# Kernel optimization log

Measured on AMD Instinct MI355X. Metric: run time of the kernel, lower is better.

Reference implementation:

```python
import jax, jax.numpy as jnp
import numpy as np

# skimage color deconvolution constants: hed_from_rgb = inv(rgb_from_hed)
_RGB_FROM_HED = np.array([[0.65, 0.70, 0.29],
                          [0.07, 0.99, 0.11],
                          [0.27, 0.57, 0.78]], dtype=np.float64)
_HED_FROM_RGB = np.linalg.inv(_RGB_FROM_HED).astype(np.float32)
_LOG_ADJUST = float(np.log(1e-6))  # skimage separate_stains log base


def setup_inputs() -> dict:
    key = jax.random.key(0)
    k1, = jax.random.split(key, 1)
    x = jax.random.uniform(k1, (64, 3, 512, 512), dtype=jnp.float32)  # RGB patches in [0,1]
    gamma = jnp.ones((1,), dtype=jnp.float32)   # InstanceNorm2d affine weight
    beta = jnp.zeros((1,), dtype=jnp.float32)   # InstanceNorm2d affine bias
    return {"x": x, "gamma": gamma, "beta": beta}


def reference(x, gamma, beta):
    h_weights = jnp.asarray(_HED_FROM_RGB[:, 0])  # only H (hematoxylin) column needed, shape (3,)

    # --- skimage.color.separate_stains, batched (replaces per-sample CPU loop) ---
    rgb = jnp.clip(x, 0.0, 1.0)                  # torch.clamp(t, 0, 1)
    rgb = jnp.maximum(rgb, 1e-6)                 # avoid log(0)
    od = jnp.log(rgb) / _LOG_ADJUST              # optical density, (B,3,H,W)
    h = jnp.einsum('bchw,c->bhw', od, h_weights) # stain matrix multiply, H channel only
    h = jnp.maximum(h, 0.0)[:, None, :, :]       # (B,1,H,W), skimage clips stains at 0

    # --- FFT magnitude spectrum ---
    fft = jnp.fft.fft2(h, norm='forward')        # complex64, scaled by 1/(H*W)
    fft = jnp.fft.fftshift(fft, axes=(-2, -1))
    mag = jnp.abs(fft)

    # --- _normalize_log_fft: log1p then per-image min-max ---
    log_mag = jnp.log1p(mag)
    mn = jnp.min(log_mag, axis=(-2, -1), keepdims=True)
    mx = jnp.max(log_mag, axis=(-2, -1), keepdims=True)
    rng = mx - mn
    safe_rng = jnp.where(rng > 0, rng, 1.0)
    normed = jnp.where(rng > 0, (log_mag - mn) / safe_rng, 0.0)

    # --- nn.InstanceNorm2d(1, affine=True), eps=1e-5 ---
    mu = jnp.mean(normed, axis=(-2, -1), keepdims=True)
    var = jnp.var(normed, axis=(-2, -1), keepdims=True)
    out = (normed - mu) * jax.lax.rsqrt(var + 1e-5)
    return out * gamma[None, :, None, None] + beta[None, :, None, None]
```

## Files before the change

kernel.cpp:

```cpp
#include <hip/hip_runtime.h>
#include <hip/hip_fp16.h>
#include <math.h>


#define PI_F 3.14159265358979323846f
#define FROW 264
#define LMSTR 264
#define LVMAX 1.6f
#define QE (65535.0f / LVMAX)
#define QD (LVMAX / 65535.0f)
#define XSTR 568

__device__ __forceinline__ int MU(int p) {
    return ((p >> 6) * 72) + (p & 56) + ((p & 7) ^ ((p >> 3) & 7));
}
__device__ __forceinline__ int odrev(int k) {
    return ((k & 7) << 6) | (k & 56) | (k >> 6);
}

__device__ __forceinline__ float2 cadd(float2 a, float2 b) { return make_float2(a.x + b.x, a.y + b.y); }
__device__ __forceinline__ float2 csub(float2 a, float2 b) { return make_float2(a.x - b.x, a.y - b.y); }
__device__ __forceinline__ float2 cmul(float2 a, float2 w) {
    return make_float2(a.x * w.x - a.y * w.y, a.x * w.y + a.y * w.x);
}

__device__ __forceinline__ void dft8(float2 v[8]) {
    const float s = 0.70710678118654752f;
    float2 a0 = cadd(v[0], v[4]), b0 = csub(v[0], v[4]);
    float2 a1 = cadd(v[1], v[5]), b1 = csub(v[1], v[5]);
    float2 a2 = cadd(v[2], v[6]), b2 = csub(v[2], v[6]);
    float2 a3 = cadd(v[3], v[7]), b3 = csub(v[3], v[7]);
    b1 = make_float2(s * (b1.x + b1.y), s * (b1.y - b1.x));
    b2 = make_float2(b2.y, -b2.x);
    b3 = make_float2(s * (b3.y - b3.x), -s * (b3.x + b3.y));
    float2 c0 = cadd(a0, a2), c1 = cadd(a1, a3);
    float2 d0 = csub(a0, a2), d1 = csub(a1, a3);
    d1 = make_float2(d1.y, -d1.x);
    v[0] = cadd(c0, c1); v[4] = csub(c0, c1);
    v[2] = cadd(d0, d1); v[6] = csub(d0, d1);
    float2 e0 = cadd(b0, b2), e1 = cadd(b1, b3);
    float2 f0 = csub(b0, b2), f1 = csub(b1, b3);
    f1 = make_float2(f1.y, -f1.x);
    v[1] = cadd(e0, e1); v[5] = csub(e0, e1);
    v[3] = cadd(f0, f1); v[7] = csub(f0, f1);
}

__device__ __forceinline__ void fft512_reg(float2* Xw, const float2* TW, int lane) {
    float2 v[8];
    #pragma unroll
    for (int m = 0; m < 8; ++m) v[m] = Xw[MU(lane + (m << 6))];
    dft8(v);
    #pragma unroll
    for (int m = 1; m < 8; ++m) v[m] = cmul(v[m], TW[(lane * m) & 511]);
    #pragma unroll
    for (int m = 0; m < 8; ++m) Xw[MU((m << 6) + lane)] = v[m];
    __builtin_amdgcn_wave_barrier();
    const int b = lane >> 3, t = lane & 7;
    const int base2 = (b << 6) + t;
    #pragma unroll
    for (int m = 0; m < 8; ++m) v[m] = Xw[MU(base2 + (m << 3))];
    dft8(v);
    #pragma unroll
    for (int m = 1; m < 8; ++m) v[m] = cmul(v[m], TW[(t * m) << 3]);
    #pragma unroll
    for (int m = 0; m < 8; ++m) Xw[MU(base2 + (m << 3))] = v[m];
    __builtin_amdgcn_wave_barrier();
    const int base3 = (b << 6) + (t << 3);
    #pragma unroll
    for (int j = 0; j < 8; ++j) v[j] = Xw[MU(base3 + j)];
    dft8(v);
    #pragma unroll
    for (int sidx = 0; sidx < 8; ++sidx) Xw[MU(base3 + sidx)] = v[sidx];
    __builtin_amdgcn_wave_barrier();
}

__device__ __forceinline__ void hstore(float2* Xw, int c,
                                       float r0v, float g0v, float b0v,
                                       float r1v, float g1v, float b1v,
                                       float w0, float w1, float w2) {
    r0v = fminf(fmaxf(r0v, 1e-6f), 1.0f);
    g0v = fminf(fmaxf(g0v, 1e-6f), 1.0f);
    b0v = fminf(fmaxf(b0v, 1e-6f), 1.0f);
    r1v = fminf(fmaxf(r1v, 1e-6f), 1.0f);
    g1v = fminf(fmaxf(g1v, 1e-6f), 1.0f);
    b1v = fminf(fmaxf(b1v, 1e-6f), 1.0f);
    float h0 = fmaxf(w0 * __log2f(r0v) + w1 * __log2f(g0v) + w2 * __log2f(b0v), 0.0f);
    float h1 = fmaxf(w0 * __log2f(r1v) + w1 * __log2f(g1v) + w2 * __log2f(b1v), 0.0f);
    Xw[MU(c)] = make_float2(h0, h1);
}

__global__ __launch_bounds__(256) void k_rowfft(const float* __restrict__ x,
                                                __half2* __restrict__ Fh,
                                                float w0, float w1, float w2) {
    const int b = blockIdx.x >> 6;
    const int p = blockIdx.x & 63;
    __shared__ float2 X[4 * XSTR];
    __shared__ float2 TW[512];
    const int tid = threadIdx.x;
    const int w = tid >> 6, lane = tid & 63;
    #pragma unroll
    for (int t = 0; t < 8; ++t) {
        int idx = lane + (t << 6);
        float sn, cs;
        __sincosf(-PI_F * (float)idx * (1.0f / 256.0f), &sn, &cs);
        TW[idx] = make_float2(cs, sn);
    }
    float2* Xw = X + w * XSTR;
    const float* xb = x + (size_t)b * 786432;
    const int r0 = (p << 3) + (w << 1);

    #pragma unroll
    for (int q = 0; q < 2; ++q) {
        const int cb = (q << 8) + (lane << 2);
        float4 R0 = *(const float4*)(xb +          (r0 << 9) + cb);
        float4 G0 = *(const float4*)(xb + 262144 + (r0 << 9) + cb);
        float4 B0 = *(const float4*)(xb + 524288 + (r0 << 9) + cb);
        float4 R1 = *(const float4*)(xb +          ((r0 + 1) << 9) + cb);
        float4 G1 = *(const float4*)(xb + 262144 + ((r0 + 1) << 9) + cb);
        float4 B1 = *(const float4*)(xb + 524288 + ((r0 + 1) << 9) + cb);
        hstore(Xw, cb + 0, R0.x, G0.x, B0.x, R1.x, G1.x, B1.x, w0, w1, w2);
        hstore(Xw, cb + 1, R0.y, G0.y, B0.y, R1.y, G1.y, B1.y, w0, w1, w2);
        hstore(Xw, cb + 2, R0.z, G0.z, B0.z, R1.z, G1.z, B1.z, w0, w1, w2);
        hstore(Xw, cb + 3, R0.w, G0.w, B0.w, R1.w, G1.w, B1.w, w0, w1, w2);
    }
    __builtin_amdgcn_wave_barrier();

    fft512_reg(Xw, TW, lane);

    __half2* Fb = Fh + (size_t)b * (512 * FROW);
    #pragma unroll
    for (int t = 0; t < 4; ++t) {
        int k = lane + (t << 6);
        int m = (512 - k) & 511;
        float2 zk = Xw[MU(odrev(k))];
        float2 zm = Xw[MU(odrev(m))];
        Fb[r0 * FROW + k]       = __floats2half2_rn(0.5f * (zk.x + zm.x),  0.5f * (zk.y - zm.y));
        Fb[(r0 + 1) * FROW + k] = __floats2half2_rn(0.5f * (zk.y + zm.y), -0.5f * (zk.x - zm.x));
    }
    if (lane == 0) {
        float2 z = Xw[MU(odrev(256))];
        Fb[r0 * FROW + 256]       = __floats2half2_rn(z.x, 0.0f);
        Fb[(r0 + 1) * FROW + 256] = __floats2half2_rn(z.y, 0.0f);
    }
}

__global__ __launch_bounds__(512) void k_colfft(const __half2* __restrict__ Fh,
                                                unsigned short* __restrict__ lmu,
                                                float4* __restrict__ partials) {
    const int b = blockIdx.x >> 4;
    const int g = blockIdx.x & 15;
    __shared__ float2 X[8 * XSTR];
    __shared__ float2 TW[512];
    __shared__ float4 wred[8];
    const int tid = threadIdx.x;
    const int w = tid >> 6, lane = tid & 63;
    {
        float sn, cs;
        __sincosf(-PI_F * (float)tid * (1.0f / 256.0f), &sn, &cs);
        TW[tid] = make_float2(cs, sn);
    }
    const __half2* Fb = Fh + (size_t)b * (512 * FROW);
    unsigned short* lm_b = lmu + (size_t)b * (512 * LMSTR);
    float mn = 1e30f, mx = -1e30f, s1 = 0.0f, s2 = 0.0f;

    for (int pass = 0; pass < 2; ++pass) {
        const int u0 = (g << 4) + (pass << 3);
        const bool packpass = (g == 0 && pass == 0);
        __syncthreads();
        for (int i = tid; i < 4096; i += 512) {
            int y = i >> 3, c = i & 7;
            float2 v;
            if (packpass && c == 0) {
                float2 f0   = __half22float2(Fb[y * FROW]);
                float2 f256 = __half22float2(Fb[y * FROW + 256]);
                v = make_float2(f0.x, f256.x);
            } else {
                v = __half22float2(Fb[y * FROW + u0 + c]);
            }
            X[c * XSTR + MU(y)] = v;
        }
        __syncthreads();
        fft512_reg(X + w * XSTR, TW, lane);
        __syncthreads();
        for (int i = tid; i < 4096; i += 512) {
            int k = i >> 3, c = i & 7;
            int ro = (k + 256) & 511;
            if (packpass && c == 0) {
                int m = (512 - k) & 511;
                float2 zk = X[MU(odrev(k))];
                float2 zm = X[MU(odrev(m))];
                float2 c0   = make_float2(0.5f * (zk.x + zm.x),  0.5f * (zk.y - zm.y));
                float2 c256 = make_float2(0.5f * (zk.y + zm.y), -0.5f * (zk.x - zm.x));
                float lv0   = __log2f(1.0f + sqrtf(c0.x * c0.x + c0.y * c0.y));
                float lv256 = __log2f(1.0f + sqrtf(c256.x * c256.x + c256.y * c256.y));
                unsigned q0 = (unsigned)__float2uint_rn(fminf(lv0,   LVMAX) * QE);
                unsigned q6 = (unsigned)__float2uint_rn(fminf(lv256, LVMAX) * QE);
                lm_b[ro * LMSTR]       = (unsigned short)q0;
                lm_b[ro * LMSTR + 256] = (unsigned short)q6;
                mn = fminf(mn, fminf(lv0, lv256));
                mx = fmaxf(mx, fmaxf(lv0, lv256));
                s1 += lv0 + lv256;
                s2 += lv0 * lv0 + lv256 * lv256;
            } else {
                int u = u0 + c;
                float2 v = X[c * XSTR + MU(odrev(k))];
                float lv = __log2f(1.0f + sqrtf(v.x * v.x + v.y * v.y));
                unsigned q = (unsigned)__float2uint_rn(fminf(lv, LVMAX) * QE);
                lm_b[ro * LMSTR + u] = (unsigned short)q;
                mn = fminf(mn, lv);
                mx = fmaxf(mx, lv);
                s1 += 2.0f * lv;
                s2 += 2.0f * lv * lv;
            }
        }
    }

    #pragma unroll
    for (int off = 32; off > 0; off >>= 1) {
        mn = fminf(mn, __shfl_down(mn, off, 64));
        mx = fmaxf(mx, __shfl_down(mx, off, 64));
        s1 += __shfl_down(s1, off, 64);
        s2 += __shfl_down(s2, off, 64);
    }
    if (lane == 0) wred[w] = make_float4(mn, mx, s1, s2);
    __syncthreads();
    if (tid == 0) {
        float4 r = wred[0];
        #pragma unroll
        for (int wv = 1; wv < 8; ++wv) {
            float4 q2 = wred[wv];
            r.x = fminf(r.x, q2.x);
            r.y = fmaxf(r.y, q2.y);
            r.z += q2.z;
            r.w += q2.w;
        }
        partials[blockIdx.x] = r;
    }
}

__global__ __launch_bounds__(64) void k_coeff(const float4* __restrict__ partials,
                                              const float* __restrict__ gamma,
                                              const float* __restrict__ beta,
                                              float2* __restrict__ coeff) {
    const int b = blockIdx.x;
    float mn = 1e30f, mx = -1e30f, s1 = 0.0f, s2 = 0.0f;
    if (threadIdx.x < 16) {
        float4 r = partials[(b << 4) + threadIdx.x];
        mn = r.x; mx = r.y; s1 = r.z; s2 = r.w;
    }
    #pragma unroll
    for (int off = 32; off > 0; off >>= 1) {
        mn = fminf(mn, __shfl_down(mn, off, 64));
        mx = fmaxf(mx, __shfl_down(mx, off, 64));
        s1 += __shfl_down(s1, off, 64);
        s2 += __shfl_down(s2, off, 64);
    }
    if (threadIdx.x == 0) {
        const float N = 262144.0f;
        float mean = s1 / N;
        float var = fmaxf(s2 / N - mean * mean, 0.0f);
        float rng = mx - mn;
        float g = gamma[0], bt = beta[0];
        float A, B;
        if (rng > 0.0f) {
            float inv = 1.0f / rng;
            float varn = var * inv * inv;
            float sc = 1.0f / sqrtf(varn + 1e-5f);
            A = g * sc * inv;
            B = bt - mean * A;
        } else {
            A = 0.0f;
            B = bt;
        }
        coeff[b] = make_float2(A, B);
    }
}

__global__ __launch_bounds__(256) void k_norm(const unsigned short* __restrict__ lmu,
                                              float* __restrict__ out,
                                              const float2* __restrict__ coeff) {
    const int p = blockIdx.x & 255;
    const int b = blockIdx.x >> 8;
    const float2 ab = coeff[b];
    const float A = ab.x, B = ab.y;
    const int rA = p;
    const int rB = (p == 0) ? 256 : 512 - p;
    const unsigned short* lb = lmu + (size_t)b * (512 * LMSTR);
    float* ob = out + ((size_t)b << 18);
    const int tid = threadIdx.x;
    #pragma unroll
    for (int hh = 0; hh < 2; ++hh) {
        const int r = hh ? rB : rA;
        const int rm = (512 - r) & 511;
        const unsigned short* Ld = lb + (size_t)r * LMSTR;
        const unsigned short* Lm = lb + (size_t)rm * LMSTR;
        float lvd = (float)Ld[tid] * QD;
        ob[(r << 9) + 256 + tid] = A * lvd + B;
        float lvm = (tid == 0) ? ((float)Ld[256] * QD)
                               : ((float)Lm[256 - tid] * QD);
        ob[(r << 9) + tid] = A * lvm + B;
    }
}

extern "C" void kernel_launch(void* const* d_in, const int* in_sizes, int n_in,
                              void* d_out, int out_size, void* d_ws, size_t ws_size,
                              hipStream_t stream) {
    const float* x     = (const float*)d_in[0];
    const float* gamma = (const float*)d_in[1];
    const float* beta  = (const float*)d_in[2];
    float* out = (float*)d_out;

    __half2* Fh = (__half2*)d_ws;
    unsigned short* lmu = (unsigned short*)((char*)d_ws + ((size_t)40 << 20));
    float4* partials = (float4*)((char*)d_ws + ((size_t)60 << 20));
    float2* coeff    = (float2*)((char*)d_ws + ((size_t)60 << 20) + 1024 * sizeof(float4));

    const double M00=0.65, M01=0.70, M02=0.29;
    const double M10=0.07, M11=0.99, M12=0.11;
    const double M20=0.27, M21=0.57, M22=0.78;
    const double det = M00*(M11*M22 - M12*M21)
                     - M01*(M10*M22 - M12*M20)
                     + M02*(M10*M21 - M11*M20);
    const float hw0 = (float)( (M11*M22 - M12*M21) / det);
    const float hw1 = (float)(-(M10*M22 - M12*M20) / det);
    const float hw2 = (float)( (M10*M21 - M11*M20) / det);
    const float invLA2 = (float)(log(2.0) / log(1e-6));
    const float sN = 1.0f / (512.0f * 512.0f);
    const float w0 = hw0 * invLA2 * sN;
    const float w1 = hw1 * invLA2 * sN;
    const float w2 = hw2 * invLA2 * sN;

    k_rowfft<<<64 * 64, 256, 0, stream>>>(x, Fh, w0, w1, w2);
    k_colfft<<<64 * 16, 512, 0, stream>>>(Fh, lmu, partials);
    k_coeff<<<64, 64, 0, stream>>>(partials, gamma, beta, coeff);
    k_norm<<<64 * 256, 256, 0, stream>>>(lmu, out, coeff);
}
```

Measured before the change: 118.3 us.

## Fuse coefficient reduction into column FFT via last-block ticket; tile normalize kernel

Removes the separate k_coeff launch by having the last k_colfft block to finish, detected with an atomic ticket and threadfence, compute the per-image normalization coefficients. A hipMemsetAsync resets the ticket before each launch. k_norm is restructured so each block stages 8 rows of quantized log-magnitude in shared memory and writes float4-vectorized outputs, cutting the block count from 16384 to 4096. This trades a kernel launch for an atomic and a memset, and the shared-memory staging adds a barrier per block.

```diff
diff --git a/kernel.cpp b/kernel.cpp
--- a/kernel.cpp
+++ b/kernel.cpp
@@ -146,12 +146,17 @@
 
 __global__ __launch_bounds__(512) void k_colfft(const __half2* __restrict__ Fh,
                                                 unsigned short* __restrict__ lmu,
-                                                float4* __restrict__ partials) {
+                                                float4* __restrict__ partials,
+                                                float2* __restrict__ coeff,
+                                                unsigned int* __restrict__ ticket,
+                                                const float* __restrict__ gamma,
+                                                const float* __restrict__ beta) {
     const int b = blockIdx.x >> 4;
     const int g = blockIdx.x & 15;
     __shared__ float2 X[8 * XSTR];
     __shared__ float2 TW[512];
     __shared__ float4 wred[8];
+    __shared__ int isLastS;
     const int tid = threadIdx.x;
     const int w = tid >> 6, lane = tid & 63;
     {
@@ -235,70 +240,95 @@
             r.w += q2.w;
         }
         partials[blockIdx.x] = r;
-    }
-}
-
-__global__ __launch_bounds__(64) void k_coeff(const float4* __restrict__ partials,
-                                              const float* __restrict__ gamma,
-                                              const float* __restrict__ beta,
-                                              float2* __restrict__ coeff) {
-    const int b = blockIdx.x;
-    float mn = 1e30f, mx = -1e30f, s1 = 0.0f, s2 = 0.0f;
-    if (threadIdx.x < 16) {
-        float4 r = partials[(b << 4) + threadIdx.x];
-        mn = r.x; mx = r.y; s1 = r.z; s2 = r.w;
-    }
-    #pragma unroll
-    for (int off = 32; off > 0; off >>= 1) {
-        mn = fminf(mn, __shfl_down(mn, off, 64));
-        mx = fmaxf(mx, __shfl_down(mx, off, 64));
-        s1 += __shfl_down(s1, off, 64);
-        s2 += __shfl_down(s2, off, 64);
-    }
-    if (threadIdx.x == 0) {
-        const float N = 262144.0f;
-        float mean = s1 / N;
-        float var = fmaxf(s2 / N - mean * mean, 0.0f);
-        float rng = mx - mn;
-        float g = gamma[0], bt = beta[0];
-        float A, B;
-        if (rng > 0.0f) {
-            float inv = 1.0f / rng;
-            float varn = var * inv * inv;
-            float sc = 1.0f / sqrtf(varn + 1e-5f);
-            A = g * sc * inv;
-            B = bt - mean * A;
-        } else {
-            A = 0.0f;
-            B = bt;
-        }
-        coeff[b] = make_float2(A, B);
+        __threadfence();
+        unsigned old = atomicAdd(ticket, 1u);
+        isLastS = (old == 1023u);
+    }
+    __syncthreads();
+    if (isLastS) {
+        __threadfence();
+        if (tid < 64) {
+            float fmn = 1e30f, fmx = -1e30f, fs1 = 0.0f, fs2 = 0.0f;
+            #pragma unroll
+            for (int k = 0; k < 16; ++k) {
+                float4 r = partials[(tid << 4) + k];
+                fmn = fminf(fmn, r.x);
+                fmx = fmaxf(fmx, r.y);
+                fs1 += r.z;
+                fs2 += r.w;
+            }
+            const float N = 262144.0f;
+            float mean = fs1 / N;
+            float var = fmaxf(fs2 / N - mean * mean, 0.0f);
+            float rng = fmx - fmn;
+            float gm = gamma[0], bt = beta[0];
+            float A, B;
+            if (rng > 0.0f) {
+                float inv = 1.0f / rng;
+                float varn = var * inv * inv;
+                float sc = 1.0f / sqrtf(varn + 1e-5f);
+                A = gm * sc * inv;
+                B = bt - mean * A;
+            } else {
+                A = 0.0f;
+                B = bt;
+            }
+            coeff[tid] = make_float2(A, B);
+        }
     }
 }
 
 __global__ __launch_bounds__(256) void k_norm(const unsigned short* __restrict__ lmu,
                                               float* __restrict__ out,
                                               const float2* __restrict__ coeff) {
-    const int p = blockIdx.x & 255;
-    const int b = blockIdx.x >> 8;
+    const int j = blockIdx.x & 63;
+    const int b = blockIdx.x >> 6;
+    __shared__ unsigned short L[8][260];
     const float2 ab = coeff[b];
     const float A = ab.x, B = ab.y;
-    const int rA = p;
-    const int rB = (p == 0) ? 256 : 512 - p;
     const unsigned short* lb = lmu + (size_t)b * (512 * LMSTR);
     float* ob = out + ((size_t)b << 18);
     const int tid = threadIdx.x;
-    #pragma unroll
-    for (int hh = 0; hh < 2; ++hh) {
-        const int r = hh ? rB : rA;
-        const int rm = (512 - r) & 511;
+
+    auto rowOf = [&](int row8) -> int {
+        int q = row8 >> 1, h = row8 & 1;
+        int p = (j << 2) + q;
+        return h ? ((p == 0) ? 256 : 512 - p) : p;
+    };
+
+    for (int i = tid; i < 8 * 65; i += 256) {
+        int row8 = i / 65, c4 = i % 65;
+        int r = rowOf(row8);
         const unsigned short* Ld = lb + (size_t)r * LMSTR;
-        const unsigned short* Lm = lb + (size_t)rm * LMSTR;
-        float lvd = (float)Ld[tid] * QD;
-        ob[(r << 9) + 256 + tid] = A * lvd + B;
-        float lvm = (tid == 0) ? ((float)Ld[256] * QD)
-                               : ((float)Lm[256 - tid] * QD);
-        ob[(r << 9) + tid] = A * lvm + B;
+        if (c4 < 64) {
+            *(uint2*)&L[row8][c4 << 2] = *(const uint2*)&Ld[c4 << 2];
+        } else {
+            L[row8][256] = Ld[256];
+        }
+    }
+    __syncthreads();
+
+    for (int i = tid; i < 1024; i += 256) {
+        int row8 = i >> 7, f4 = i & 127;
+        int co = f4 << 2;
+        int r = rowOf(row8);
+        int p = (j << 2) + (row8 >> 1);
+        int m8 = (p == 0) ? row8 : (row8 ^ 1);
+        float4 o;
+        if (f4 >= 64) {
+            int u = co - 256;
+            o.x = (float)L[row8][u]     * QD * A + B;
+            o.y = (float)L[row8][u + 1] * QD * A + B;
+            o.z = (float)L[row8][u + 2] * QD * A + B;
+            o.w = (float)L[row8][u + 3] * QD * A + B;
+        } else {
+            o.x = ((co == 0) ? (float)L[row8][256]
+                             : (float)L[m8][256 - co]) * QD * A + B;
+            o.y = (float)L[m8][255 - co] * QD * A + B;
+            o.z = (float)L[m8][254 - co] * QD * A + B;
+            o.w = (float)L[m8][253 - co] * QD * A + B;
+        }
+        *(float4*)&ob[(r << 9) + co] = o;
     }
 }
 
@@ -313,7 +343,10 @@
     __half2* Fh = (__half2*)d_ws;
     unsigned short* lmu = (unsigned short*)((char*)d_ws + ((size_t)40 << 20));
     float4* partials = (float4*)((char*)d_ws + ((size_t)60 << 20));
-    float2* coeff    = (float2*)((char*)d_ws + ((size_t)60 << 20) + 1024 * sizeof(float4));
+    float2* coeff    = (float2*)((char*)d_ws + ((size_t)60 << 20) + 16384);
+    unsigned int* ticket = (unsigned int*)((char*)d_ws + ((size_t)60 << 20) + 32768);
+
+    hipMemsetAsync(ticket, 0, 4, stream);
 
     const double M00=0.65, M01=0.70, M02=0.29;
     const double M10=0.07, M11=0.99, M12=0.11;
@@ -331,7 +364,7 @@
     const float w2 = hw2 * invLA2 * sN;
 
     k_rowfft<<<64 * 64, 256, 0, stream>>>(x, Fh, w0, w1, w2);
-    k_colfft<<<64 * 16, 512, 0, stream>>>(Fh, lmu, partials);
-    k_coeff<<<64, 64, 0, stream>>>(partials, gamma, beta, coeff);
-    k_norm<<<64 * 256, 256, 0, stream>>>(lmu, out, coeff);
-}
+    k_colfft<<<64 * 16, 512, 0, stream>>>(Fh, lmu, partials, coeff, ticket,
+                                          gamma, beta);
+    k_norm<<<64 * 64, 256, 0, stream>>>(lmu, out, coeff);
+}
```

After: 151.5 us. +28.0%, slower.
